# Kernel optimization log

Hardware: AMD Instinct MI355X
Metric: run time of the kernel (lower is better)

The kernel has to match this reference:

```python
import jax, jax.numpy as jnp
import numpy as np

CX, CY, FX, FY = 334.081, 169.808, 460.585, 460.268
EPS = 1e-07
T_ITER = 1000
MIN_POINTS = 5000
H, W, B = 360, 640, 2


def _point_cloud(depth_img):
    # depth_img: [C,H,W]; channel 2 if C==3 else channel 0
    depth = depth_img[2] if depth_img.shape[0] == 3 else depth_img[0]
    rows, cols = depth.shape
    c = jnp.arange(cols, dtype=depth.dtype)[None, :]
    r = jnp.arange(rows, dtype=depth.dtype)[:, None]
    valid = (depth > 0) & (depth < 65535)
    nanv = jnp.float32(jnp.nan)
    z = jnp.where(valid, depth / 1000.0, nanv)
    x = jnp.where(valid, z * (c - CX) / FX, nanv)
    y = jnp.where(valid, z * (r - CY) / FY, nanv)
    pcd = jnp.stack([x.ravel(), y.ravel(), z.ravel()], axis=1)  # [N,3]
    return pcd, valid.ravel()


def setup_inputs() -> dict:
    key = jax.random.key(0)
    k1, k2 = jax.random.split(key)
    fake = jax.random.uniform(k1, (B, 1, H, W), dtype=jnp.float32)
    real = jax.random.uniform(k2, (B, 1, H, W), dtype=jnp.float32)
    return {"fake": fake, "real": real, "epoch": 5, "show_image": 0}


def _forward(fake, real, epoch):
    real_pcd, vr = _point_cloud(real[0])
    fake_pcd, vf = _point_cloud(fake[0])
    real_pcd = real_pcd * 1000.0
    fake_pcd = fake_pcd * 1000.0
    # pcd[pcd==0] = eps  (NaN==0 is False, NaNs preserved)
    real_pcd = jnp.where(real_pcd == 0, EPS, real_pcd)
    fake_pcd = jnp.where(fake_pcd == 0, EPS, fake_pcd)

    # combined validity mask (real-valid then fake-valid filtering chain)
    m = vr & vf
    cnt = jnp.maximum(jnp.sum(m), 1)

    def sel(v, fill):
        return jnp.where(m, v, fill)

    def mrmse(a, b):
        d = sel(a, 0.0) - sel(b, 0.0)
        return jnp.sqrt(jnp.sum(d * d) / cnt)

    lossX = mrmse(real_pcd[:, 0], fake_pcd[:, 0])
    lossY = mrmse(real_pcd[:, 1], fake_pcd[:, 1])
    lossZ = mrmse(real_pcd[:, 2], fake_pcd[:, 2])
    dlog = jnp.log(jnp.abs(sel(real_pcd[:, 2], 1.0))) - jnp.log(jnp.abs(sel(fake_pcd[:, 2], 1.0)))
    RMSE_log = 10000.0 * jnp.sqrt(jnp.sum(jnp.where(m, dlog * dlog, 0.0)) / cnt)
    loss17 = RMSE_log * jnp.abs(10.0 * (3.0 - jnp.exp(lossX) - jnp.exp(lossY) - jnp.exp(lossZ)))

    # ---- batched RANSAC plane fit on normalized fake cloud ----
    nan_cloud = jnp.where(jnp.isnan(fake_pcd), 0.0, fake_pcd)
    pts = nan_cloud / jnp.max(nan_cloud)  # [N,3]
    N = pts.shape[0]
    thresh = jnp.maximum(jnp.float32(0.025 - 0.001 * epoch), jnp.float32(0.005))

    rkey = jax.random.key(42)
    idx = jax.random.randint(rkey, (T_ITER, 3), 0, N)  # 3 sample points per trial
    p = pts[idx]  # [T,3,3]
    vA = p[:, 1] - p[:, 0]
    vB = p[:, 2] - p[:, 0]
    nrm = jnp.cross(vA, vB)
    nrm = nrm / jnp.linalg.norm(nrm, axis=1, keepdims=True)  # unit normals [T,3]
    kk = -jnp.sum(nrm * p[:, 1], axis=1)  # plane offsets [T]
    dist = pts @ nrm.T + kk[None, :]  # [N,T], |n|=1 so no extra divide
    inl = jnp.abs(dist) <= thresh  # [N,T]
    counts = jnp.sum(inl, axis=0)  # [T]
    # keep first trial with strictly-largest count among counts > minPoints
    score = jnp.where(counts > MIN_POINTS, counts, -1)
    best = jnp.argmax(score)
    a, b, c, d = nrm[best, 0], nrm[best, 1], nrm[best, 2], kk[best]
    inlier_mask = inl[:, best]  # [N]

    # translation/rotation were built via torch.tensor(...) -> detached in torch
    trans = jax.lax.stop_gradient(jnp.stack([jnp.zeros(()), jnp.zeros(()), d / c]))
    n2 = a * a + b * b + c * c
    cos_t = c / jnp.sqrt(n2)
    sin_t = jnp.sqrt((a * a + b * b) / n2)
    sab = jnp.sqrt(a * a + b * b)
    u1 = b / sab
    u2 = -a / sab
    R = jnp.stack([
        jnp.stack([cos_t + u1 * u1 * (1 - cos_t), u1 * u2 * (1 - cos_t), u2 * sin_t]),
        jnp.stack([u1 * u2 * (1 - cos_t), cos_t + u2 * u2 * (1 - cos_t), -u1 * sin_t]),
        jnp.stack([-u2 * sin_t, u1 * sin_t, cos_t]),
    ])
    Rt = jax.lax.stop_gradient(R).T  # torch transposes before matmul

    plane_pts = pts + trans
    zc = (plane_pts @ Rt)[:, 2]  # rotated z for all points; inliers selected by mask
    icnt = jnp.maximum(jnp.sum(inlier_mask), 1)
    zmax = jnp.max(jnp.where(inlier_mask, zc, -jnp.inf))
    zmin = jnp.min(jnp.where(inlier_mask, zc, jnp.inf))
    below = jnp.sum(jnp.where(inlier_mask, jnp.abs(zc - zmax), 0.0)) / icnt
    above = jnp.sum(jnp.where(inlier_mask, jnp.abs(zc - zmin), 0.0)) / icnt
    above = jnp.where(above == 0, jnp.float32(1e-07), above)
    plane_mean_dist_grad = 1000.0 * (above + below)

    loss_curv = loss17 + plane_mean_dist_grad
    delta = jnp.stack([RMSE_log, lossX, lossY, lossZ, plane_mean_dist_grad, loss17])
    return delta, loss_curv


def reference(fake, real, epoch, show_image):
    del show_image  # unused in the loss math
    return _forward(fake, real, epoch)
```

## Files before the change

kernel.cpp:

```cpp
#include <hip/hip_runtime.h>

namespace {

typedef float v2f __attribute__((ext_vector_type(2)));

constexpr int kW = 640;
constexpr int kN = 230400;
constexpr unsigned kSpan = 230400u;
constexpr int kB1 = 900;
constexpr int kB3 = 1024;
constexpr int kPPB3 = 225;
constexpr int kB5 = 900;
constexpr unsigned kPoison = 0xAAAAAAAAu;

struct __align__(16) Acc {
  double lossX, lossY, lossZ, rmse_log, loss17;
  float maxv;
  unsigned selkey;
};

constexpr size_t kOffAcc     = 0;
constexpr size_t kOffC1      = 256;
constexpr size_t kOffC3      = 320;
constexpr size_t kOffC5      = 384;
constexpr size_t kOffPlanes  = 512;
constexpr size_t kOffSP      = 512 + 16384;
constexpr size_t kOffZP      = kOffSP + 43200;
constexpr size_t kOffPartial = kOffZP + 28800;
constexpr size_t kOffPts     = kOffPartial + (size_t)kB3 * 256 * 4;

__device__ __forceinline__ void ast64(unsigned long long* p, unsigned long long v) {
  __hip_atomic_store(p, v, __ATOMIC_RELAXED, __HIP_MEMORY_SCOPE_AGENT);
}
__device__ __forceinline__ unsigned long long ald64(const unsigned long long* p) {
  return __hip_atomic_load(p, __ATOMIC_RELAXED, __HIP_MEMORY_SCOPE_AGENT);
}
__device__ __forceinline__ void ast32(unsigned* p, unsigned v) {
  __hip_atomic_store(p, v, __ATOMIC_RELAXED, __HIP_MEMORY_SCOPE_AGENT);
}
__device__ __forceinline__ unsigned ald32(const unsigned* p) {
  return __hip_atomic_load(p, __ATOMIC_RELAXED, __HIP_MEMORY_SCOPE_AGENT);
}

__device__ __forceinline__ unsigned rotl32(unsigned v, int r) {
  return (v << r) | (v >> (32 - r));
}

__device__ __forceinline__ void threefry(unsigned c0, unsigned c1,
                                         unsigned& o0, unsigned& o1) {
  const unsigned ks0 = 0u, ks1 = 42u, ks2 = 0x1BD11BDAu ^ 0u ^ 42u;
  unsigned x0 = c0 + ks0, x1 = c1 + ks1;
#define TFR(r) { x0 += x1; x1 = rotl32(x1, (r)); x1 ^= x0; }
  TFR(13) TFR(15) TFR(26) TFR(6)
  x0 += ks1; x1 += ks2 + 1u;
  TFR(17) TFR(29) TFR(16) TFR(24)
  x0 += ks2; x1 += ks0 + 2u;
  TFR(13) TFR(15) TFR(26) TFR(6)
  x0 += ks0; x1 += ks1 + 3u;
  TFR(17) TFR(29) TFR(16) TFR(24)
  x0 += ks1; x1 += ks2 + 4u;
  TFR(13) TFR(15) TFR(26) TFR(6)
  x0 += ks2; x1 += ks0 + 5u;
#undef TFR
  o0 = x0; o1 = x1;
}

__device__ __forceinline__ void pix_coords(float d, int row, int col, bool& valid,
                                           float& x, float& y, float& z) {
  valid = (d > 0.0f) && (d < 65535.0f);
  float z0 = d / 1000.0f;
  float x0 = z0 * ((float)col - 334.081f) / 460.585f;
  float y0 = z0 * ((float)row - 169.808f) / 460.268f;
  x = x0 * 1000.0f;
  y = y0 * 1000.0f;
  z = z0 * 1000.0f;
  if (x == 0.0f) x = 1e-7f;
  if (y == 0.0f) y = 1e-7f;
  if (z == 0.0f) z = 1e-7f;
}

__device__ __forceinline__ void make_pt(float d, int row, int col, float maxv,
                                        float& x, float& y, float& z) {
  bool v; float a, b, c;
  pix_coords(d, row, col, v, a, b, c);
  x = (v ? a : 0.f) / maxv;
  y = (v ? b : 0.f) / maxv;
  z = (v ? c : 0.f) / maxv;
}

__device__ __forceinline__ float get_thresh(int ep) {
  return (float)fmax(0.025 - 0.001 * (double)ep, 0.005);
}

__global__ __launch_bounds__(256) void k_stats(const float* __restrict__ fake,
                                               const float* __restrict__ real,
                                               float* __restrict__ out,
                                               char* __restrict__ ws) {
  Acc* acc = (Acc*)(ws + kOffAcc);
  unsigned* ctr = (unsigned*)(ws + kOffC1);
  float4* planes = (float4*)(ws + kOffPlanes);
  unsigned long long* sp = (unsigned long long*)(ws + kOffSP);
  float4* ptsraw = (float4*)(ws + kOffPts);

  const int b = blockIdx.x, t = threadIdx.x;
  const int lane = t & 63, wid = t >> 6;

  __shared__ double sD0[4], sD1[4], sD2[4], sD3[4];
  __shared__ int sI0[4];
  __shared__ float sF0[4];
  __shared__ unsigned sArr;
  __shared__ float sMaxv;

  {
    int i = b * 256 + t;
    int row = i / kW, col = i - row * kW;
    bool vr, vf; float rx, ry, rz, fx, fy, fz;
    pix_coords(real[i], row, col, vr, rx, ry, rz);
    pix_coords(fake[i], row, col, vf, fx, fy, fz);
    ptsraw[i] = make_float4(vf ? fx : 0.f, vf ? fy : 0.f, vf ? fz : 0.f, 0.f);
    double dx2 = 0, dy2 = 0, dz2 = 0, dl2 = 0; int cc = 0;
    if (vr && vf) {
      float ddx = rx - fx, ddy = ry - fy, ddz = rz - fz;
      dx2 = (double)ddx * (double)ddx;
      dy2 = (double)ddy * (double)ddy;
      dz2 = (double)ddz * (double)ddz;
      double dl = log(fabs((double)rz)) - log(fabs((double)fz));
      dl2 = dl * dl;
      cc = 1;
    }
    float mx = vf ? fmaxf(fmaxf(fx, fy), fz) : 0.0f;
    for (int o = 32; o; o >>= 1) {
      dx2 += __shfl_down(dx2, o); dy2 += __shfl_down(dy2, o);
      dz2 += __shfl_down(dz2, o); dl2 += __shfl_down(dl2, o);
      cc += __shfl_down(cc, o);
      mx = fmaxf(mx, __shfl_down(mx, o));
    }
    if (lane == 0) { sD0[wid]=dx2; sD1[wid]=dy2; sD2[wid]=dz2; sD3[wid]=dl2;
                     sI0[wid]=cc; sF0[wid]=mx; }
    __syncthreads();
    if (t == 0) {
      unsigned long long* e = sp + (size_t)b * 6;
      ast64(e + 0, __double_as_longlong(sD0[0]+sD0[1]+sD0[2]+sD0[3]));
      ast64(e + 1, __double_as_longlong(sD1[0]+sD1[1]+sD1[2]+sD1[3]));
      ast64(e + 2, __double_as_longlong(sD2[0]+sD2[1]+sD2[2]+sD2[3]));
      ast64(e + 3, __double_as_longlong(sD3[0]+sD3[1]+sD3[2]+sD3[3]));
      ast64(e + 4, (unsigned long long)(sI0[0]+sI0[1]+sI0[2]+sI0[3]));
      float bm = fmaxf(fmaxf(sF0[0], sF0[1]), fmaxf(sF0[2], sF0[3]));
      ast64(e + 5, (unsigned long long)__float_as_uint(bm));
    }
  }
  __syncthreads();
  if (t == 0)
    sArr = __hip_atomic_fetch_add(ctr, 1u, __ATOMIC_RELAXED, __HIP_MEMORY_SCOPE_AGENT);
  __syncthreads();
  if (sArr != kPoison + (unsigned)(kB1 - 1)) return;

  {
    double gx = 0, gy = 0, gz = 0, gl = 0; int gc = 0; float gm = 0.f;
    for (int r = t; r < kB1; r += 256) {
      const unsigned long long* e = sp + (size_t)r * 6;
      gx += __longlong_as_double(ald64(e + 0));
      gy += __longlong_as_double(ald64(e + 1));
      gz += __longlong_as_double(ald64(e + 2));
      gl += __longlong_as_double(ald64(e + 3));
      gc += (int)ald64(e + 4);
      gm = fmaxf(gm, __uint_as_float((unsigned)ald64(e + 5)));
    }
    for (int o = 32; o; o >>= 1) {
      gx += __shfl_down(gx, o); gy += __shfl_down(gy, o);
      gz += __shfl_down(gz, o); gl += __shfl_down(gl, o);
      gc += __shfl_down(gc, o);
      gm = fmaxf(gm, __shfl_down(gm, o));
    }
    if (lane == 0) { sD0[wid]=gx; sD1[wid]=gy; sD2[wid]=gz; sD3[wid]=gl;
                     sI0[wid]=gc; sF0[wid]=gm; }
    __syncthreads();
    if (t == 0) {
      double SX = sD0[0]+sD0[1]+sD0[2]+sD0[3];
      double SY = sD1[0]+sD1[1]+sD1[2]+sD1[3];
      double SZ = sD2[0]+sD2[1]+sD2[2]+sD2[3];
      double SL = sD3[0]+sD3[1]+sD3[2]+sD3[3];
      int CN = sI0[0]+sI0[1]+sI0[2]+sI0[3];
      float MX = fmaxf(fmaxf(sF0[0], sF0[1]), fmaxf(sF0[2], sF0[3]));
      double cntd = (CN > 0) ? (double)CN : 1.0;
      double lossX = sqrt(SX / cntd);
      double lossY = sqrt(SY / cntd);
      double lossZ = sqrt(SZ / cntd);
      double rmse_log = 10000.0 * sqrt(SL / cntd);
      double loss17 = rmse_log * fabs(10.0 * (3.0 - exp(lossX) - exp(lossY) - exp(lossZ)));
      acc->lossX = lossX; acc->lossY = lossY; acc->lossZ = lossZ;
      acc->rmse_log = rmse_log; acc->loss17 = loss17;
      acc->maxv = MX;
      acc->selkey = 0u;
      out[0] = (float)rmse_log;
      out[1] = (float)lossX;
      out[2] = (float)lossY;
      out[3] = (float)lossZ;
      out[5] = (float)loss17;
      sMaxv = MX;
    }
    __syncthreads();
  }
  {
    float maxv = sMaxv;
#pragma unroll
    for (int j = 0; j < 4; j++) {
      int pid = t * 4 + j;
      if (pid < 1000) {
        float px[3], py[3], pz[3];
#pragma unroll
        for (int v = 0; v < 3; v++) {
          unsigned p = 3u * (unsigned)pid + (unsigned)v;
          unsigned o0, o1;
          threefry(p, p + 3000u, o0, o1);
          unsigned idx = o1 % kSpan;
          int row = (int)(idx / kW), col = (int)idx - row * kW;
          make_pt(fake[idx], row, col, maxv, px[v], py[v], pz[v]);
        }
        float ax = px[1]-px[0], ay = py[1]-py[0], az = pz[1]-pz[0];
        float bx = px[2]-px[0], by = py[2]-py[0], bz = pz[2]-pz[0];
        float nx = ay*bz - az*by;
        float ny = az*bx - ax*bz;
        float nz = ax*by - ay*bx;
        float nn = sqrtf(nx*nx + ny*ny + nz*nz);
        nx /= nn; ny /= nn; nz /= nn;
        float kk = -(nx*px[1] + ny*py[1] + nz*pz[1]);
        planes[pid] = make_float4(nx, ny, nz, kk);
      } else {
        planes[pid] = make_float4(0.f, 0.f, 0.f, 3e38f);
      }
    }
  }
}

__global__ __launch_bounds__(256) void k_count(const int* __restrict__ epoch,
                                               char* __restrict__ ws) {
  Acc* acc = (Acc*)(ws + kOffAcc);
  unsigned* ctr = (unsigned*)(ws + kOffC3);
  const float4* planes = (const float4*)(ws + kOffPlanes);
  unsigned* partial = (unsigned*)(ws + kOffPartial);
  const float4* ptsraw = (const float4*)(ws + kOffPts);

  const int b = blockIdx.x, t = threadIdx.x;
  const float th = get_thresh(*epoch);
  const float maxv = acc->maxv;

  __shared__ float4 sPts[kPPB3];
  __shared__ uint4 sAcc[16][16];
  __shared__ unsigned sArr;

  if (t < kPPB3) {
    float4 r = ptsraw[b * kPPB3 + t];
    sPts[t] = make_float4(r.x / maxv, r.y / maxv, r.z / maxv, 0.f);
  }
  float4 p0 = planes[t * 4 + 0], p1 = planes[t * 4 + 1];
  float4 p2 = planes[t * 4 + 2], p3 = planes[t * 4 + 3];
  v2f Ax = {p0.x, p1.x}, Ay = {p0.y, p1.y}, Az = {p0.z, p1.z}, Aw = {p0.w, p1.w};
  v2f Bx = {p2.x, p3.x}, By = {p2.y, p3.y}, Bz = {p2.z, p3.z}, Bw = {p2.w, p3.w};
  __syncthreads();

  int c0 = 0, c1 = 0, c2 = 0, c3 = 0;
#pragma unroll 5
  for (int s = 0; s < kPPB3; ++s) {
    float4 q = sPts[s];
    v2f qx = {q.x, q.x}, qy = {q.y, q.y}, qz = {q.z, q.z};
    v2f dA = __builtin_elementwise_fma(qx, Ax,
             __builtin_elementwise_fma(qy, Ay,
             __builtin_elementwise_fma(qz, Az, Aw)));
    v2f dB = __builtin_elementwise_fma(qx, Bx,
             __builtin_elementwise_fma(qy, By,
             __builtin_elementwise_fma(qz, Bz, Bw)));
    c0 += (fabsf(dA.x) <= th) ? 1 : 0;
    c1 += (fabsf(dA.y) <= th) ? 1 : 0;
    c2 += (fabsf(dB.x) <= th) ? 1 : 0;
    c3 += (fabsf(dB.y) <= th) ? 1 : 0;
  }
  ast32(&partial[b * 256 + t],
        (unsigned)c0 | ((unsigned)c1 << 8) | ((unsigned)c2 << 16) | ((unsigned)c3 << 24));

  __syncthreads();
  if (t == 0)
    sArr = __hip_atomic_fetch_add(ctr, 1u, __ATOMIC_RELAXED, __HIP_MEMORY_SCOPE_AGENT);
  __syncthreads();
  unsigned ret = sArr;
  if (ret < kPoison + (unsigned)(kB3 - 16)) return;

  int r = (int)(ret - (kPoison + (unsigned)(kB3 - 16)));
  if (t == 0) {
    while (ald32(ctr) != kPoison + (unsigned)kB3) __builtin_amdgcn_s_sleep(2);
  }
  __syncthreads();

  int owner = r * 16 + (t & 15);
  int chunk = t >> 4;
  unsigned s0 = 0, s1 = 0, s2 = 0, s3 = 0;
  for (int row = chunk * 64; row < chunk * 64 + 64; ++row) {
    unsigned v = ald32(&partial[row * 256 + owner]);
    s0 += v & 0xFFu; s1 += (v >> 8) & 0xFFu;
    s2 += (v >> 16) & 0xFFu; s3 += (v >> 24) & 0xFFu;
  }
  sAcc[t & 15][chunk] = make_uint4(s0, s1, s2, s3);
  __syncthreads();

  unsigned mykey = 0u;
  if (t < 16) {
    unsigned t0 = 0, t1 = 0, t2 = 0, t3 = 0;
    for (int j = 0; j < 16; ++j) {
      uint4 v = sAcc[t][j];
      t0 += v.x; t1 += v.y; t2 += v.z; t3 += v.w;
    }
    unsigned tot[4] = {t0, t1, t2, t3};
    int pbase = (r * 16 + t) * 4;
#pragma unroll
    for (int k = 0; k < 4; ++k) {
      int p = pbase + k;
      if (p < 1000) {
        int score = ((int)tot[k] > 5000) ? (int)tot[k] : -1;
        unsigned key = ((unsigned)(score + 2) << 10) | (unsigned)(1023 - p);
        mykey = key > mykey ? key : mykey;
      }
    }
  }
  for (int o = 32; o; o >>= 1) {
    unsigned other = __shfl_down(mykey, o);
    mykey = other > mykey ? other : mykey;
  }
  if (t == 0) atomicMax(&acc->selkey, mykey);
}

__global__ __launch_bounds__(256) void k_zc(const int* __restrict__ epoch,
                                            float* __restrict__ out,
                                            char* __restrict__ ws) {
  Acc* acc = (Acc*)(ws + kOffAcc);
  unsigned* ctr = (unsigned*)(ws + kOffC5);
  const float4* planes = (const float4*)(ws + kOffPlanes);
  unsigned long long* zp = (unsigned long long*)(ws + kOffZP);
  const float4* ptsraw = (const float4*)(ws + kOffPts);

  const int b = blockIdx.x, t = threadIdx.x;
  const int lane = t & 63, wid = t >> 6;
  const float th = get_thresh(*epoch);
  const float maxv = acc->maxv;

  int best = 1023 - (int)(acc->selkey & 1023u);
  float4 pl = planes[best];
  const float a = pl.x, bb = pl.y, c = pl.z, d = pl.w;
  float n2 = a * a + bb * bb + c * c;
  float cos_t = c / sqrtf(n2);
  float sin_t = sqrtf((a * a + bb * bb) / n2);
  float sab = sqrtf(a * a + bb * bb);
  float u1 = bb / sab, u2 = -a / sab;
  const float r0 = -u2 * sin_t, r1 = u1 * sin_t, r2 = cos_t, tz = d / c;

  __shared__ double sD0[4];
  __shared__ int sI0[4];
  __shared__ float sF0[4], sF1[4];
  __shared__ unsigned sArr;

  double sz = 0.0; int ic = 0; float zmx = -INFINITY, zmn = -INFINITY;
  {
    float4 rw = ptsraw[b * 256 + t];
    float qx = rw.x / maxv, qy = rw.y / maxv, qz = rw.z / maxv;
    float dist = fmaf(qx, a, fmaf(qy, bb, fmaf(qz, c, d)));
    if (fabsf(dist) <= th) {
      float zc = fmaf(qx, r0, fmaf(qy, r1, (qz + tz) * r2));
      sz = (double)zc; ic = 1; zmx = zc; zmn = -zc;
    }
  }
  for (int o = 32; o; o >>= 1) {
    sz += __shfl_down(sz, o); ic += __shfl_down(ic, o);
    zmx = fmaxf(zmx, __shfl_down(zmx, o));
    zmn = fmaxf(zmn, __shfl_down(zmn, o));
  }
  if (lane == 0) { sD0[wid] = sz; sI0[wid] = ic; sF0[wid] = zmx; sF1[wid] = zmn; }
  __syncthreads();
  if (t == 0) {
    unsigned long long* e = zp + (size_t)b * 4;
    ast64(e + 0, __double_as_longlong(sD0[0]+sD0[1]+sD0[2]+sD0[3]));
    ast64(e + 1, (unsigned long long)(sI0[0]+sI0[1]+sI0[2]+sI0[3]));
    float bmx = fmaxf(fmaxf(sF0[0], sF0[1]), fmaxf(sF0[2], sF0[3]));
    float bmn = fmaxf(fmaxf(sF1[0], sF1[1]), fmaxf(sF1[2], sF1[3]));
    ast64(e + 2, (unsigned long long)__float_as_uint(bmx) |
                 ((unsigned long long)__float_as_uint(bmn) << 32));
  }
  __syncthreads();
  if (t == 0)
    sArr = __hip_atomic_fetch_add(ctr, 1u, __ATOMIC_RELAXED, __HIP_MEMORY_SCOPE_AGENT);
  __syncthreads();
  if (sArr != kPoison + (unsigned)(kB5 - 1)) return;

  {
    double gs = 0.0; int gi = 0; float gmx = -INFINITY, gmn = -INFINITY;
    for (int r = t; r < kB5; r += 256) {
      const unsigned long long* e = zp + (size_t)r * 4;
      gs += __longlong_as_double(ald64(e + 0));
      gi += (int)ald64(e + 1);
      unsigned long long mm = ald64(e + 2);
      gmx = fmaxf(gmx, __uint_as_float((unsigned)(mm & 0xFFFFFFFFu)));
      gmn = fmaxf(gmn, __uint_as_float((unsigned)(mm >> 32)));
    }
    for (int o = 32; o; o >>= 1) {
      gs += __shfl_down(gs, o); gi += __shfl_down(gi, o);
      gmx = fmaxf(gmx, __shfl_down(gmx, o));
      gmn = fmaxf(gmn, __shfl_down(gmn, o));
    }
    if (lane == 0) { sD0[wid] = gs; sI0[wid] = gi; sF0[wid] = gmx; sF1[wid] = gmn; }
    __syncthreads();
    if (t == 0) {
      double S = sD0[0]+sD0[1]+sD0[2]+sD0[3];
      int IC = sI0[0]+sI0[1]+sI0[2]+sI0[3];
      float MX = fmaxf(fmaxf(sF0[0], sF0[1]), fmaxf(sF0[2], sF0[3]));
      float MN = fmaxf(fmaxf(sF1[0], sF1[1]), fmaxf(sF1[2], sF1[3]));
      double below = 0.0, above = 0.0;
      if (IC > 0) {
        double icd = (double)IC;
        double mean = S / icd;
        below = (double)MX - mean;
        above = mean - (double)(-MN);
      }
      if (above == 0.0) above = 1e-7;
      double pmdg = 1000.0 * (above + below);
      out[4] = (float)pmdg;
      out[6] = (float)(acc->loss17 + pmdg);
    }
  }
}

}

extern "C" void kernel_launch(void* const* d_in, const int* in_sizes, int n_in,
                              void* d_out, int out_size, void* d_ws, size_t ws_size,
                              hipStream_t stream) {
  (void)in_sizes; (void)n_in; (void)out_size; (void)ws_size;
  const float* fake = (const float*)d_in[0];
  const float* real = (const float*)d_in[1];
  const int* epoch = (const int*)d_in[2];
  float* out = (float*)d_out;
  char* ws = (char*)d_ws;

  k_stats<<<kB1, 256, 0, stream>>>(fake, real, out, ws);
  k_count<<<kB3, 256, 0, stream>>>(epoch, ws);
  k_zc<<<kB5, 256, 0, stream>>>(epoch, out, ws);
}
```

Before: 135.6 us.

## Fuse three kernels into one persistent kernel with grid-wide flag synchronization

Merges the stats, RANSAC inlier-count and plane-z kernels into one kernel of 512 blocks, each owning 450 pixels kept in shared memory across all phases. The global point buffer and two extra launches go away. Blocks now spin on global flags (plane-ready, selection-done), so the design relies on all 512 blocks being co-resident, with launch bounds set to two blocks per SM. Partial counts are widened to 16-bit fields since each block now covers more points.

```diff
diff --git a/kernel.cpp b/kernel.cpp
--- a/kernel.cpp
+++ b/kernel.cpp
@@ -5,29 +5,21 @@
 typedef float v2f __attribute__((ext_vector_type(2)));
 
 constexpr int kW = 640;
-constexpr int kN = 230400;
 constexpr unsigned kSpan = 230400u;
-constexpr int kB1 = 900;
-constexpr int kB3 = 1024;
-constexpr int kPPB3 = 225;
-constexpr int kB5 = 900;
+constexpr int kB = 512;
+constexpr int kPPB = 450;
 constexpr unsigned kPoison = 0xAAAAAAAAu;
 
-struct __align__(16) Acc {
-  double lossX, lossY, lossZ, rmse_log, loss17;
-  float maxv;
-  unsigned selkey;
-};
-
 constexpr size_t kOffAcc     = 0;
-constexpr size_t kOffC1      = 256;
-constexpr size_t kOffC3      = 320;
-constexpr size_t kOffC5      = 384;
-constexpr size_t kOffPlanes  = 512;
-constexpr size_t kOffSP      = 512 + 16384;
-constexpr size_t kOffZP      = kOffSP + 43200;
-constexpr size_t kOffPartial = kOffZP + 28800;
-constexpr size_t kOffPts     = kOffPartial + (size_t)kB3 * 256 * 4;
+constexpr size_t kOffCA      = 256;
+constexpr size_t kOffCB      = 320;
+constexpr size_t kOffCSel    = 384;
+constexpr size_t kOffCC      = 448;
+constexpr size_t kOffFlagPl  = 512;
+constexpr size_t kOffPlanes  = 1024;
+constexpr size_t kOffSP      = kOffPlanes + 16384;
+constexpr size_t kOffZP      = kOffSP + 24576;
+constexpr size_t kOffPartial = kOffZP + 16384;
 
 __device__ __forceinline__ void ast64(unsigned long long* p, unsigned long long v) {
   __hip_atomic_store(p, v, __ATOMIC_RELAXED, __HIP_MEMORY_SCOPE_AGENT);
@@ -40,6 +32,23 @@
 }
 __device__ __forceinline__ unsigned ald32(const unsigned* p) {
   return __hip_atomic_load(p, __ATOMIC_RELAXED, __HIP_MEMORY_SCOPE_AGENT);
+}
+__device__ __forceinline__ void ast32rel(unsigned* p, unsigned v) {
+  __hip_atomic_store(p, v, __ATOMIC_RELEASE, __HIP_MEMORY_SCOPE_AGENT);
+}
+__device__ __forceinline__ unsigned ald32acq(const unsigned* p) {
+  return __hip_atomic_load(p, __ATOMIC_ACQUIRE, __HIP_MEMORY_SCOPE_AGENT);
+}
+
+__device__ __forceinline__ float lo_f(unsigned long long v) {
+  return __uint_as_float((unsigned)(v & 0xFFFFFFFFull));
+}
+__device__ __forceinline__ float hi_f(unsigned long long v) {
+  return __uint_as_float((unsigned)(v >> 32));
+}
+__device__ __forceinline__ unsigned long long pack_f2(float lo, float hi) {
+  return (unsigned long long)__float_as_uint(lo) |
+         ((unsigned long long)__float_as_uint(hi) << 32);
 }
 
 __device__ __forceinline__ unsigned rotl32(unsigned v, int r) {
@@ -92,43 +101,57 @@
   return (float)fmax(0.025 - 0.001 * (double)ep, 0.005);
 }
 
-__global__ __launch_bounds__(256) void k_stats(const float* __restrict__ fake,
-                                               const float* __restrict__ real,
-                                               float* __restrict__ out,
-                                               char* __restrict__ ws) {
-  Acc* acc = (Acc*)(ws + kOffAcc);
-  unsigned* ctr = (unsigned*)(ws + kOffC1);
-  float4* planes = (float4*)(ws + kOffPlanes);
+__global__ __launch_bounds__(256, 2) void k_fused(const float* __restrict__ fake,
+                                                  const float* __restrict__ real,
+                                                  const int* __restrict__ epoch,
+                                                  float* __restrict__ out,
+                                                  char* __restrict__ ws) {
+  unsigned* maxvBits = (unsigned*)(ws + kOffAcc);
+  unsigned long long* loss17p = (unsigned long long*)(ws + kOffAcc + 8);
+  unsigned* selkeyp = (unsigned*)(ws + kOffAcc + 16);
+  unsigned* ctrA = (unsigned*)(ws + kOffCA);
+  unsigned* ctrB = (unsigned*)(ws + kOffCB);
+  unsigned* ctrSel = (unsigned*)(ws + kOffCSel);
+  unsigned* ctrC = (unsigned*)(ws + kOffCC);
+  unsigned* flagPl = (unsigned*)(ws + kOffFlagPl);
+  unsigned long long* planes64 = (unsigned long long*)(ws + kOffPlanes);
   unsigned long long* sp = (unsigned long long*)(ws + kOffSP);
-  float4* ptsraw = (float4*)(ws + kOffPts);
+  unsigned long long* zp = (unsigned long long*)(ws + kOffZP);
+  unsigned long long* partial = (unsigned long long*)(ws + kOffPartial);
 
   const int b = blockIdx.x, t = threadIdx.x;
   const int lane = t & 63, wid = t >> 6;
-
+  const float th = get_thresh(*epoch);
+
+  __shared__ float4 sPts[kPPB];
   __shared__ double sD0[4], sD1[4], sD2[4], sD3[4];
   __shared__ int sI0[4];
-  __shared__ float sF0[4];
+  __shared__ float sF0[4], sF1[4];
+  __shared__ uint4 sAcc[16][16];
   __shared__ unsigned sArr;
   __shared__ float sMaxv;
+  __shared__ unsigned long long sPl[2];
 
   {
-    int i = b * 256 + t;
-    int row = i / kW, col = i - row * kW;
-    bool vr, vf; float rx, ry, rz, fx, fy, fz;
-    pix_coords(real[i], row, col, vr, rx, ry, rz);
-    pix_coords(fake[i], row, col, vf, fx, fy, fz);
-    ptsraw[i] = make_float4(vf ? fx : 0.f, vf ? fy : 0.f, vf ? fz : 0.f, 0.f);
-    double dx2 = 0, dy2 = 0, dz2 = 0, dl2 = 0; int cc = 0;
-    if (vr && vf) {
-      float ddx = rx - fx, ddy = ry - fy, ddz = rz - fz;
-      dx2 = (double)ddx * (double)ddx;
-      dy2 = (double)ddy * (double)ddy;
-      dz2 = (double)ddz * (double)ddz;
-      double dl = log(fabs((double)rz)) - log(fabs((double)fz));
-      dl2 = dl * dl;
-      cc = 1;
-    }
-    float mx = vf ? fmaxf(fmaxf(fx, fy), fz) : 0.0f;
+    double dx2 = 0, dy2 = 0, dz2 = 0, dl2 = 0; int cc = 0; float mx = 0.f;
+    for (int k = t; k < kPPB; k += 256) {
+      const int i = b * kPPB + k;
+      const int row = i / kW, col = i - row * kW;
+      bool vr, vf; float rx, ry, rz, fxx, fyy, fzz;
+      pix_coords(real[i], row, col, vr, rx, ry, rz);
+      pix_coords(fake[i], row, col, vf, fxx, fyy, fzz);
+      sPts[k] = make_float4(vf ? fxx : 0.f, vf ? fyy : 0.f, vf ? fzz : 0.f, 0.f);
+      if (vr && vf) {
+        float ddx = rx - fxx, ddy = ry - fyy, ddz = rz - fzz;
+        dx2 += (double)ddx * (double)ddx;
+        dy2 += (double)ddy * (double)ddy;
+        dz2 += (double)ddz * (double)ddz;
+        double dl = log(fabs((double)rz)) - log(fabs((double)fzz));
+        dl2 += dl * dl;
+        cc += 1;
+      }
+      mx = fmaxf(mx, vf ? fmaxf(fmaxf(fxx, fyy), fzz) : 0.f);
+    }
     for (int o = 32; o; o >>= 1) {
       dx2 += __shfl_down(dx2, o); dy2 += __shfl_down(dy2, o);
       dz2 += __shfl_down(dz2, o); dl2 += __shfl_down(dl2, o);
@@ -151,247 +174,245 @@
   }
   __syncthreads();
   if (t == 0)
-    sArr = __hip_atomic_fetch_add(ctr, 1u, __ATOMIC_RELAXED, __HIP_MEMORY_SCOPE_AGENT);
-  __syncthreads();
-  if (sArr != kPoison + (unsigned)(kB1 - 1)) return;
+    sArr = __hip_atomic_fetch_add(ctrA, 1u, __ATOMIC_RELAXED, __HIP_MEMORY_SCOPE_AGENT);
+  __syncthreads();
+
+  if (sArr == kPoison + (unsigned)(kB - 1)) {
+    {
+      double gx = 0, gy = 0, gz = 0, gl = 0; int gc = 0; float gm = 0.f;
+      for (int r = t; r < kB; r += 256) {
+        const unsigned long long* e = sp + (size_t)r * 6;
+        gx += __longlong_as_double(ald64(e + 0));
+        gy += __longlong_as_double(ald64(e + 1));
+        gz += __longlong_as_double(ald64(e + 2));
+        gl += __longlong_as_double(ald64(e + 3));
+        gc += (int)ald64(e + 4);
+        gm = fmaxf(gm, __uint_as_float((unsigned)ald64(e + 5)));
+      }
+      for (int o = 32; o; o >>= 1) {
+        gx += __shfl_down(gx, o); gy += __shfl_down(gy, o);
+        gz += __shfl_down(gz, o); gl += __shfl_down(gl, o);
+        gc += __shfl_down(gc, o);
+        gm = fmaxf(gm, __shfl_down(gm, o));
+      }
+      if (lane == 0) { sD0[wid]=gx; sD1[wid]=gy; sD2[wid]=gz; sD3[wid]=gl;
+                       sI0[wid]=gc; sF0[wid]=gm; }
+      __syncthreads();
+      if (t == 0) {
+        double SX = sD0[0]+sD0[1]+sD0[2]+sD0[3];
+        double SY = sD1[0]+sD1[1]+sD1[2]+sD1[3];
+        double SZ = sD2[0]+sD2[1]+sD2[2]+sD2[3];
+        double SL = sD3[0]+sD3[1]+sD3[2]+sD3[3];
+        int CN = sI0[0]+sI0[1]+sI0[2]+sI0[3];
+        float MX = fmaxf(fmaxf(sF0[0], sF0[1]), fmaxf(sF0[2], sF0[3]));
+        double cntd = (CN > 0) ? (double)CN : 1.0;
+        double lossX = sqrt(SX / cntd);
+        double lossY = sqrt(SY / cntd);
+        double lossZ = sqrt(SZ / cntd);
+        double rmse_log = 10000.0 * sqrt(SL / cntd);
+        double loss17 = rmse_log * fabs(10.0 * (3.0 - exp(lossX) - exp(lossY) - exp(lossZ)));
+        ast32(maxvBits, __float_as_uint(MX));
+        ast64(loss17p, __double_as_longlong(loss17));
+        ast32(selkeyp, 0u);
+        out[0] = (float)rmse_log;
+        out[1] = (float)lossX;
+        out[2] = (float)lossY;
+        out[3] = (float)lossZ;
+        out[5] = (float)loss17;
+        sMaxv = MX;
+      }
+      __syncthreads();
+    }
+    {
+      float maxv = sMaxv;
+#pragma unroll
+      for (int j = 0; j < 4; j++) {
+        int pid = t * 4 + j;
+        if (pid < 1000) {
+          float px[3], py[3], pz[3];
+#pragma unroll
+          for (int v = 0; v < 3; v++) {
+            unsigned p = 3u * (unsigned)pid + (unsigned)v;
+            unsigned o0, o1;
+            threefry(p, p + 3000u, o0, o1);
+            unsigned idx = o1 % kSpan;
+            int row = (int)(idx / kW), col = (int)idx - row * kW;
+            make_pt(fake[idx], row, col, maxv, px[v], py[v], pz[v]);
+          }
+          float ax = px[1]-px[0], ay = py[1]-py[0], az = pz[1]-pz[0];
+          float bx = px[2]-px[0], by = py[2]-py[0], bz = pz[2]-pz[0];
+          float nx = ay*bz - az*by;
+          float ny = az*bx - ax*bz;
+          float nz = ax*by - ay*bx;
+          float nn = sqrtf(nx*nx + ny*ny + nz*nz);
+          nx /= nn; ny /= nn; nz /= nn;
+          float kk = -(nx*px[1] + ny*py[1] + nz*pz[1]);
+          ast64(planes64 + 2*pid,     pack_f2(nx, ny));
+          ast64(planes64 + 2*pid + 1, pack_f2(nz, kk));
+        } else {
+          ast64(planes64 + 2*pid,     pack_f2(0.f, 0.f));
+          ast64(planes64 + 2*pid + 1, pack_f2(0.f, 3e38f));
+        }
+      }
+    }
+    __syncthreads();
+    if (t == 0) ast32rel(flagPl, 1u);
+  }
+
+  if (t == 0) {
+    while (ald32acq(flagPl) != 1u) __builtin_amdgcn_s_sleep(2);
+    sMaxv = __uint_as_float(ald32(maxvBits));
+  }
+  __syncthreads();
+  const float maxv = sMaxv;
 
   {
-    double gx = 0, gy = 0, gz = 0, gl = 0; int gc = 0; float gm = 0.f;
-    for (int r = t; r < kB1; r += 256) {
-      const unsigned long long* e = sp + (size_t)r * 6;
-      gx += __longlong_as_double(ald64(e + 0));
-      gy += __longlong_as_double(ald64(e + 1));
-      gz += __longlong_as_double(ald64(e + 2));
-      gl += __longlong_as_double(ald64(e + 3));
-      gc += (int)ald64(e + 4);
-      gm = fmaxf(gm, __uint_as_float((unsigned)ald64(e + 5)));
+    float4 pl[4];
+#pragma unroll
+    for (int j = 0; j < 4; j++) {
+      unsigned long long w0 = ald64(planes64 + 2 * (t * 4 + j));
+      unsigned long long w1 = ald64(planes64 + 2 * (t * 4 + j) + 1);
+      pl[j] = make_float4(lo_f(w0), hi_f(w0), lo_f(w1), hi_f(w1));
+    }
+    for (int k = t; k < kPPB; k += 256) {
+      float4 r = sPts[k];
+      sPts[k] = make_float4(r.x / maxv, r.y / maxv, r.z / maxv, 0.f);
+    }
+    v2f Ax = {pl[0].x, pl[1].x}, Ay = {pl[0].y, pl[1].y},
+        Az = {pl[0].z, pl[1].z}, Aw = {pl[0].w, pl[1].w};
+    v2f Bx = {pl[2].x, pl[3].x}, By = {pl[2].y, pl[3].y},
+        Bz = {pl[2].z, pl[3].z}, Bw = {pl[2].w, pl[3].w};
+    __syncthreads();
+
+    int c0 = 0, c1 = 0, c2 = 0, c3 = 0;
+#pragma unroll 5
+    for (int s = 0; s < kPPB; ++s) {
+      float4 q = sPts[s];
+      v2f qx = {q.x, q.x}, qy = {q.y, q.y}, qz = {q.z, q.z};
+      v2f dA = __builtin_elementwise_fma(qx, Ax,
+               __builtin_elementwise_fma(qy, Ay,
+               __builtin_elementwise_fma(qz, Az, Aw)));
+      v2f dB = __builtin_elementwise_fma(qx, Bx,
+               __builtin_elementwise_fma(qy, By,
+               __builtin_elementwise_fma(qz, Bz, Bw)));
+      c0 += (fabsf(dA.x) <= th) ? 1 : 0;
+      c1 += (fabsf(dA.y) <= th) ? 1 : 0;
+      c2 += (fabsf(dB.x) <= th) ? 1 : 0;
+      c3 += (fabsf(dB.y) <= th) ? 1 : 0;
+    }
+    ast64(&partial[(size_t)b * 256 + t],
+          (unsigned long long)(unsigned)c0 |
+          ((unsigned long long)(unsigned)c1 << 16) |
+          ((unsigned long long)(unsigned)c2 << 32) |
+          ((unsigned long long)(unsigned)c3 << 48));
+  }
+  __syncthreads();
+  if (t == 0)
+    sArr = __hip_atomic_fetch_add(ctrB, 1u, __ATOMIC_RELAXED, __HIP_MEMORY_SCOPE_AGENT);
+  __syncthreads();
+  {
+    unsigned ret = sArr;
+    if (ret >= kPoison + (unsigned)(kB - 16)) {
+      int r = (int)(ret - (kPoison + (unsigned)(kB - 16)));
+      if (t == 0) {
+        while (ald32(ctrB) != kPoison + (unsigned)kB) __builtin_amdgcn_s_sleep(2);
+      }
+      __syncthreads();
+
+      int owner = r * 16 + (t & 15);
+      int chunk = t >> 4;
+      unsigned s0 = 0, s1 = 0, s2 = 0, s3 = 0;
+      for (int row = chunk * 32; row < chunk * 32 + 32; ++row) {
+        unsigned long long v = ald64(&partial[(size_t)row * 256 + owner]);
+        s0 += (unsigned)(v & 0xFFFFu);         s1 += (unsigned)((v >> 16) & 0xFFFFu);
+        s2 += (unsigned)((v >> 32) & 0xFFFFu); s3 += (unsigned)((v >> 48) & 0xFFFFu);
+      }
+      sAcc[t & 15][chunk] = make_uint4(s0, s1, s2, s3);
+      __syncthreads();
+
+      unsigned mykey = 0u;
+      if (t < 16) {
+        unsigned t0 = 0, t1 = 0, t2 = 0, t3 = 0;
+        for (int j = 0; j < 16; ++j) {
+          uint4 v = sAcc[t][j];
+          t0 += v.x; t1 += v.y; t2 += v.z; t3 += v.w;
+        }
+        unsigned tot[4] = {t0, t1, t2, t3};
+        int pbase = (r * 16 + t) * 4;
+#pragma unroll
+        for (int k = 0; k < 4; ++k) {
+          int p = pbase + k;
+          if (p < 1000) {
+            int score = ((int)tot[k] > 5000) ? (int)tot[k] : -1;
+            unsigned key = ((unsigned)(score + 2) << 10) | (unsigned)(1023 - p);
+            mykey = key > mykey ? key : mykey;
+          }
+        }
+      }
+      for (int o = 32; o; o >>= 1) {
+        unsigned other = __shfl_down(mykey, o);
+        mykey = other > mykey ? other : mykey;
+      }
+      if (t == 0) {
+        atomicMax(selkeyp, mykey);
+        __hip_atomic_fetch_add(ctrSel, 1u, __ATOMIC_RELEASE, __HIP_MEMORY_SCOPE_AGENT);
+      }
+    }
+  }
+  if (t == 0) {
+    while (ald32acq(ctrSel) != kPoison + 16u) __builtin_amdgcn_s_sleep(2);
+    unsigned sk = ald32(selkeyp);
+    int best = 1023 - (int)(sk & 1023u);
+    sPl[0] = ald64(planes64 + 2 * best);
+    sPl[1] = ald64(planes64 + 2 * best + 1);
+  }
+  __syncthreads();
+
+  {
+    const float a = lo_f(sPl[0]), bb = hi_f(sPl[0]);
+    const float c = lo_f(sPl[1]), d = hi_f(sPl[1]);
+    float n2 = a * a + bb * bb + c * c;
+    float cos_t = c / sqrtf(n2);
+    float sin_t = sqrtf((a * a + bb * bb) / n2);
+    float sab = sqrtf(a * a + bb * bb);
+    float u1 = bb / sab, u2 = -a / sab;
+    const float r0 = -u2 * sin_t, r1 = u1 * sin_t, r2v = cos_t, tz = d / c;
+
+    double sz = 0.0; int ic = 0; float zmx = -INFINITY, zmn = -INFINITY;
+    for (int k = t; k < kPPB; k += 256) {
+      float4 q = sPts[k];
+      float dist = fmaf(q.x, a, fmaf(q.y, bb, fmaf(q.z, c, d)));
+      if (fabsf(dist) <= th) {
+        float zc = fmaf(q.x, r0, fmaf(q.y, r1, (q.z + tz) * r2v));
+        sz += (double)zc; ic += 1; zmx = fmaxf(zmx, zc); zmn = fmaxf(zmn, -zc);
+      }
     }
     for (int o = 32; o; o >>= 1) {
-      gx += __shfl_down(gx, o); gy += __shfl_down(gy, o);
-      gz += __shfl_down(gz, o); gl += __shfl_down(gl, o);
-      gc += __shfl_down(gc, o);
-      gm = fmaxf(gm, __shfl_down(gm, o));
-    }
-    if (lane == 0) { sD0[wid]=gx; sD1[wid]=gy; sD2[wid]=gz; sD3[wid]=gl;
-                     sI0[wid]=gc; sF0[wid]=gm; }
+      sz += __shfl_down(sz, o); ic += __shfl_down(ic, o);
+      zmx = fmaxf(zmx, __shfl_down(zmx, o));
+      zmn = fmaxf(zmn, __shfl_down(zmn, o));
+    }
+    if (lane == 0) { sD0[wid] = sz; sI0[wid] = ic; sF0[wid] = zmx; sF1[wid] = zmn; }
     __syncthreads();
     if (t == 0) {
-      double SX = sD0[0]+sD0[1]+sD0[2]+sD0[3];
-      double SY = sD1[0]+sD1[1]+sD1[2]+sD1[3];
-      double SZ = sD2[0]+sD2[1]+sD2[2]+sD2[3];
-      double SL = sD3[0]+sD3[1]+sD3[2]+sD3[3];
-      int CN = sI0[0]+sI0[1]+sI0[2]+sI0[3];
-      float MX = fmaxf(fmaxf(sF0[0], sF0[1]), fmaxf(sF0[2], sF0[3]));
-      double cntd = (CN > 0) ? (double)CN : 1.0;
-      double lossX = sqrt(SX / cntd);
-      double lossY = sqrt(SY / cntd);
-      double lossZ = sqrt(SZ / cntd);
-      double rmse_log = 10000.0 * sqrt(SL / cntd);
-      double loss17 = rmse_log * fabs(10.0 * (3.0 - exp(lossX) - exp(lossY) - exp(lossZ)));
-      acc->lossX = lossX; acc->lossY = lossY; acc->lossZ = lossZ;
-      acc->rmse_log = rmse_log; acc->loss17 = loss17;
-      acc->maxv = MX;
-      acc->selkey = 0u;
-      out[0] = (float)rmse_log;
-      out[1] = (float)lossX;
-      out[2] = (float)lossY;
-      out[3] = (float)lossZ;
-      out[5] = (float)loss17;
-      sMaxv = MX;
-    }
-    __syncthreads();
-  }
-  {
-    float maxv = sMaxv;
-#pragma unroll
-    for (int j = 0; j < 4; j++) {
-      int pid = t * 4 + j;
-      if (pid < 1000) {
-        float px[3], py[3], pz[3];
-#pragma unroll
-        for (int v = 0; v < 3; v++) {
-          unsigned p = 3u * (unsigned)pid + (unsigned)v;
-          unsigned o0, o1;
-          threefry(p, p + 3000u, o0, o1);
-          unsigned idx = o1 % kSpan;
-          int row = (int)(idx / kW), col = (int)idx - row * kW;
-          make_pt(fake[idx], row, col, maxv, px[v], py[v], pz[v]);
-        }
-        float ax = px[1]-px[0], ay = py[1]-py[0], az = pz[1]-pz[0];
-        float bx = px[2]-px[0], by = py[2]-py[0], bz = pz[2]-pz[0];
-        float nx = ay*bz - az*by;
-        float ny = az*bx - ax*bz;
-        float nz = ax*by - ay*bx;
-        float nn = sqrtf(nx*nx + ny*ny + nz*nz);
-        nx /= nn; ny /= nn; nz /= nn;
-        float kk = -(nx*px[1] + ny*py[1] + nz*pz[1]);
-        planes[pid] = make_float4(nx, ny, nz, kk);
-      } else {
-        planes[pid] = make_float4(0.f, 0.f, 0.f, 3e38f);
-      }
-    }
-  }
-}
-
-__global__ __launch_bounds__(256) void k_count(const int* __restrict__ epoch,
-                                               char* __restrict__ ws) {
-  Acc* acc = (Acc*)(ws + kOffAcc);
-  unsigned* ctr = (unsigned*)(ws + kOffC3);
-  const float4* planes = (const float4*)(ws + kOffPlanes);
-  unsigned* partial = (unsigned*)(ws + kOffPartial);
-  const float4* ptsraw = (const float4*)(ws + kOffPts);
-
-  const int b = blockIdx.x, t = threadIdx.x;
-  const float th = get_thresh(*epoch);
-  const float maxv = acc->maxv;
-
-  __shared__ float4 sPts[kPPB3];
-  __shared__ uint4 sAcc[16][16];
-  __shared__ unsigned sArr;
-
-  if (t < kPPB3) {
-    float4 r = ptsraw[b * kPPB3 + t];
-    sPts[t] = make_float4(r.x / maxv, r.y / maxv, r.z / maxv, 0.f);
-  }
-  float4 p0 = planes[t * 4 + 0], p1 = planes[t * 4 + 1];
-  float4 p2 = planes[t * 4 + 2], p3 = planes[t * 4 + 3];
-  v2f Ax = {p0.x, p1.x}, Ay = {p0.y, p1.y}, Az = {p0.z, p1.z}, Aw = {p0.w, p1.w};
-  v2f Bx = {p2.x, p3.x}, By = {p2.y, p3.y}, Bz = {p2.z, p3.z}, Bw = {p2.w, p3.w};
-  __syncthreads();
-
-  int c0 = 0, c1 = 0, c2 = 0, c3 = 0;
-#pragma unroll 5
-  for (int s = 0; s < kPPB3; ++s) {
-    float4 q = sPts[s];
-    v2f qx = {q.x, q.x}, qy = {q.y, q.y}, qz = {q.z, q.z};
-    v2f dA = __builtin_elementwise_fma(qx, Ax,
-             __builtin_elementwise_fma(qy, Ay,
-             __builtin_elementwise_fma(qz, Az, Aw)));
-    v2f dB = __builtin_elementwise_fma(qx, Bx,
-             __builtin_elementwise_fma(qy, By,
-             __builtin_elementwise_fma(qz, Bz, Bw)));
-    c0 += (fabsf(dA.x) <= th) ? 1 : 0;
-    c1 += (fabsf(dA.y) <= th) ? 1 : 0;
-    c2 += (fabsf(dB.x) <= th) ? 1 : 0;
-    c3 += (fabsf(dB.y) <= th) ? 1 : 0;
-  }
-  ast32(&partial[b * 256 + t],
-        (unsigned)c0 | ((unsigned)c1 << 8) | ((unsigned)c2 << 16) | ((unsigned)c3 << 24));
-
+      unsigned long long* e = zp + (size_t)b * 4;
+      ast64(e + 0, __double_as_longlong(sD0[0]+sD0[1]+sD0[2]+sD0[3]));
+      ast64(e + 1, (unsigned long long)(sI0[0]+sI0[1]+sI0[2]+sI0[3]));
+      float bmx = fmaxf(fmaxf(sF0[0], sF0[1]), fmaxf(sF0[2], sF0[3]));
+      float bmn = fmaxf(fmaxf(sF1[0], sF1[1]), fmaxf(sF1[2], sF1[3]));
+      ast64(e + 2, (unsigned long long)__float_as_uint(bmx) |
+                   ((unsigned long long)__float_as_uint(bmn) << 32));
+    }
+  }
   __syncthreads();
   if (t == 0)
-    sArr = __hip_atomic_fetch_add(ctr, 1u, __ATOMIC_RELAXED, __HIP_MEMORY_SCOPE_AGENT);
-  __syncthreads();
-  unsigned ret = sArr;
-  if (ret < kPoison + (unsigned)(kB3 - 16)) return;
-
-  int r = (int)(ret - (kPoison + (unsigned)(kB3 - 16)));
-  if (t == 0) {
-    while (ald32(ctr) != kPoison + (unsigned)kB3) __builtin_amdgcn_s_sleep(2);
-  }
-  __syncthreads();
-
-  int owner = r * 16 + (t & 15);
-  int chunk = t >> 4;
-  unsigned s0 = 0, s1 = 0, s2 = 0, s3 = 0;
-  for (int row = chunk * 64; row < chunk * 64 + 64; ++row) {
-    unsigned v = ald32(&partial[row * 256 + owner]);
-    s0 += v & 0xFFu; s1 += (v >> 8) & 0xFFu;
-    s2 += (v >> 16) & 0xFFu; s3 += (v >> 24) & 0xFFu;
-  }
-  sAcc[t & 15][chunk] = make_uint4(s0, s1, s2, s3);
-  __syncthreads();
-
-  unsigned mykey = 0u;
-  if (t < 16) {
-    unsigned t0 = 0, t1 = 0, t2 = 0, t3 = 0;
-    for (int j = 0; j < 16; ++j) {
-      uint4 v = sAcc[t][j];
-      t0 += v.x; t1 += v.y; t2 += v.z; t3 += v.w;
-    }
-    unsigned tot[4] = {t0, t1, t2, t3};
-    int pbase = (r * 16 + t) * 4;
-#pragma unroll
-    for (int k = 0; k < 4; ++k) {
-      int p = pbase + k;
-      if (p < 1000) {
-        int score = ((int)tot[k] > 5000) ? (int)tot[k] : -1;
-        unsigned key = ((unsigned)(score + 2) << 10) | (unsigned)(1023 - p);
-        mykey = key > mykey ? key : mykey;
-      }
-    }
-  }
-  for (int o = 32; o; o >>= 1) {
-    unsigned other = __shfl_down(mykey, o);
-    mykey = other > mykey ? other : mykey;
-  }
-  if (t == 0) atomicMax(&acc->selkey, mykey);
-}
-
-__global__ __launch_bounds__(256) void k_zc(const int* __restrict__ epoch,
-                                            float* __restrict__ out,
-                                            char* __restrict__ ws) {
-  Acc* acc = (Acc*)(ws + kOffAcc);
-  unsigned* ctr = (unsigned*)(ws + kOffC5);
-  const float4* planes = (const float4*)(ws + kOffPlanes);
-  unsigned long long* zp = (unsigned long long*)(ws + kOffZP);
-  const float4* ptsraw = (const float4*)(ws + kOffPts);
-
-  const int b = blockIdx.x, t = threadIdx.x;
-  const int lane = t & 63, wid = t >> 6;
-  const float th = get_thresh(*epoch);
-  const float maxv = acc->maxv;
-
-  int best = 1023 - (int)(acc->selkey & 1023u);
-  float4 pl = planes[best];
-  const float a = pl.x, bb = pl.y, c = pl.z, d = pl.w;
-  float n2 = a * a + bb * bb + c * c;
-  float cos_t = c / sqrtf(n2);
-  float sin_t = sqrtf((a * a + bb * bb) / n2);
-  float sab = sqrtf(a * a + bb * bb);
-  float u1 = bb / sab, u2 = -a / sab;
-  const float r0 = -u2 * sin_t, r1 = u1 * sin_t, r2 = cos_t, tz = d / c;
-
-  __shared__ double sD0[4];
-  __shared__ int sI0[4];
-  __shared__ float sF0[4], sF1[4];
-  __shared__ unsigned sArr;
-
-  double sz = 0.0; int ic = 0; float zmx = -INFINITY, zmn = -INFINITY;
-  {
-    float4 rw = ptsraw[b * 256 + t];
-    float qx = rw.x / maxv, qy = rw.y / maxv, qz = rw.z / maxv;
-    float dist = fmaf(qx, a, fmaf(qy, bb, fmaf(qz, c, d)));
-    if (fabsf(dist) <= th) {
-      float zc = fmaf(qx, r0, fmaf(qy, r1, (qz + tz) * r2));
-      sz = (double)zc; ic = 1; zmx = zc; zmn = -zc;
-    }
-  }
-  for (int o = 32; o; o >>= 1) {
-    sz += __shfl_down(sz, o); ic += __shfl_down(ic, o);
-    zmx = fmaxf(zmx, __shfl_down(zmx, o));
-    zmn = fmaxf(zmn, __shfl_down(zmn, o));
-  }
-  if (lane == 0) { sD0[wid] = sz; sI0[wid] = ic; sF0[wid] = zmx; sF1[wid] = zmn; }
-  __syncthreads();
-  if (t == 0) {
-    unsigned long long* e = zp + (size_t)b * 4;
-    ast64(e + 0, __double_as_longlong(sD0[0]+sD0[1]+sD0[2]+sD0[3]));
-    ast64(e + 1, (unsigned long long)(sI0[0]+sI0[1]+sI0[2]+sI0[3]));
-    float bmx = fmaxf(fmaxf(sF0[0], sF0[1]), fmaxf(sF0[2], sF0[3]));
-    float bmn = fmaxf(fmaxf(sF1[0], sF1[1]), fmaxf(sF1[2], sF1[3]));
-    ast64(e + 2, (unsigned long long)__float_as_uint(bmx) |
-                 ((unsigned long long)__float_as_uint(bmn) << 32));
-  }
-  __syncthreads();
-  if (t == 0)
-    sArr = __hip_atomic_fetch_add(ctr, 1u, __ATOMIC_RELAXED, __HIP_MEMORY_SCOPE_AGENT);
-  __syncthreads();
-  if (sArr != kPoison + (unsigned)(kB5 - 1)) return;
+    sArr = __hip_atomic_fetch_add(ctrC, 1u, __ATOMIC_RELAXED, __HIP_MEMORY_SCOPE_AGENT);
+  __syncthreads();
+  if (sArr != kPoison + (unsigned)(kB - 1)) return;
 
   {
     double gs = 0.0; int gi = 0; float gmx = -INFINITY, gmn = -INFINITY;
-    for (int r = t; r < kB5; r += 256) {
+    for (int r = t; r < kB; r += 256) {
       const unsigned long long* e = zp + (size_t)r * 4;
       gs += __longlong_as_double(ald64(e + 0));
       gi += (int)ald64(e + 1);
@@ -420,8 +441,9 @@
       }
       if (above == 0.0) above = 1e-7;
       double pmdg = 1000.0 * (above + below);
+      double loss17 = __longlong_as_double(ald64(loss17p));
       out[4] = (float)pmdg;
-      out[6] = (float)(acc->loss17 + pmdg);
+      out[6] = (float)(loss17 + pmdg);
     }
   }
 }
@@ -438,7 +460,5 @@
   float* out = (float*)d_out;
   char* ws = (char*)d_ws;
 
-  k_stats<<<kB1, 256, 0, stream>>>(fake, real, out, ws);
-  k_count<<<kB3, 256, 0, stream>>>(epoch, ws);
-  k_zc<<<kB5, 256, 0, stream>>>(epoch, out, ws);
-}
+  k_fused<<<kB, 256, 0, stream>>>(fake, real, epoch, out, ws);
+}
```

New measurement: 205.2 us. 1.51x slower.

## Spread RANSAC plane generation across the last five arriving stats blocks

Applied to the files above, without the earlier changes.

The single last-arriving block in k_stats used to do two serial jobs: the final loss reduction and generating all 1000 candidate planes at four per thread. Now the last five blocks to arrive split this tail. One block does the loss reduction, and the other four each build 256 planes after spin-waiting until every block has arrived. The global max is now gathered with an atomicMax on float bits instead of a per-block slot plus reduction. This relies on the poisoned workspace initial value being a negative int and on all blocks being resident at once for the spin-wait.

```diff
diff --git a/kernel.cpp b/kernel.cpp
--- a/kernel.cpp
+++ b/kernel.cpp
@@ -5,7 +5,6 @@
 typedef float v2f __attribute__((ext_vector_type(2)));
 
 constexpr int kW = 640;
-constexpr int kN = 230400;
 constexpr unsigned kSpan = 230400u;
 constexpr int kB1 = 900;
 constexpr int kB3 = 1024;
@@ -13,13 +12,9 @@
 constexpr int kB5 = 900;
 constexpr unsigned kPoison = 0xAAAAAAAAu;
 
-struct __align__(16) Acc {
-  double lossX, lossY, lossZ, rmse_log, loss17;
-  float maxv;
-  unsigned selkey;
-};
-
-constexpr size_t kOffAcc     = 0;
+constexpr size_t kOffMaxv    = 0;
+constexpr size_t kOffL17     = 8;
+constexpr size_t kOffSel     = 16;
 constexpr size_t kOffC1      = 256;
 constexpr size_t kOffC3      = 320;
 constexpr size_t kOffC5      = 384;
@@ -96,7 +91,9 @@
                                                const float* __restrict__ real,
                                                float* __restrict__ out,
                                                char* __restrict__ ws) {
-  Acc* acc = (Acc*)(ws + kOffAcc);
+  int* maxvBits = (int*)(ws + kOffMaxv);
+  unsigned long long* loss17p = (unsigned long long*)(ws + kOffL17);
+  unsigned* selkeyp = (unsigned*)(ws + kOffSel);
   unsigned* ctr = (unsigned*)(ws + kOffC1);
   float4* planes = (float4*)(ws + kOffPlanes);
   unsigned long long* sp = (unsigned long long*)(ws + kOffSP);
@@ -109,7 +106,7 @@
   __shared__ int sI0[4];
   __shared__ float sF0[4];
   __shared__ unsigned sArr;
-  __shared__ float sMaxv;
+  __shared__ unsigned sMvU;
 
   {
     int i = b * 256 + t;
@@ -146,17 +143,19 @@
       ast64(e + 3, __double_as_longlong(sD3[0]+sD3[1]+sD3[2]+sD3[3]));
       ast64(e + 4, (unsigned long long)(sI0[0]+sI0[1]+sI0[2]+sI0[3]));
       float bm = fmaxf(fmaxf(sF0[0], sF0[1]), fmaxf(sF0[2], sF0[3]));
-      ast64(e + 5, (unsigned long long)__float_as_uint(bm));
+      atomicMax(maxvBits, (int)__float_as_uint(bm));
     }
   }
   __syncthreads();
   if (t == 0)
     sArr = __hip_atomic_fetch_add(ctr, 1u, __ATOMIC_RELAXED, __HIP_MEMORY_SCOPE_AGENT);
   __syncthreads();
-  if (sArr != kPoison + (unsigned)(kB1 - 1)) return;
-
-  {
-    double gx = 0, gy = 0, gz = 0, gl = 0; int gc = 0; float gm = 0.f;
+  unsigned ret = sArr;
+  if (ret < kPoison + (unsigned)(kB1 - 5)) return;
+  int role = (int)(ret - (kPoison + (unsigned)(kB1 - 5)));
+
+  if (role == 4) {
+    double gx = 0, gy = 0, gz = 0, gl = 0; int gc = 0;
     for (int r = t; r < kB1; r += 256) {
       const unsigned long long* e = sp + (size_t)r * 6;
       gx += __longlong_as_double(ald64(e + 0));
@@ -164,16 +163,13 @@
       gz += __longlong_as_double(ald64(e + 2));
       gl += __longlong_as_double(ald64(e + 3));
       gc += (int)ald64(e + 4);
-      gm = fmaxf(gm, __uint_as_float((unsigned)ald64(e + 5)));
     }
     for (int o = 32; o; o >>= 1) {
       gx += __shfl_down(gx, o); gy += __shfl_down(gy, o);
       gz += __shfl_down(gz, o); gl += __shfl_down(gl, o);
       gc += __shfl_down(gc, o);
-      gm = fmaxf(gm, __shfl_down(gm, o));
-    }
-    if (lane == 0) { sD0[wid]=gx; sD1[wid]=gy; sD2[wid]=gz; sD3[wid]=gl;
-                     sI0[wid]=gc; sF0[wid]=gm; }
+    }
+    if (lane == 0) { sD0[wid]=gx; sD1[wid]=gy; sD2[wid]=gz; sD3[wid]=gl; sI0[wid]=gc; }
     __syncthreads();
     if (t == 0) {
       double SX = sD0[0]+sD0[1]+sD0[2]+sD0[3];
@@ -181,61 +177,57 @@
       double SZ = sD2[0]+sD2[1]+sD2[2]+sD2[3];
       double SL = sD3[0]+sD3[1]+sD3[2]+sD3[3];
       int CN = sI0[0]+sI0[1]+sI0[2]+sI0[3];
-      float MX = fmaxf(fmaxf(sF0[0], sF0[1]), fmaxf(sF0[2], sF0[3]));
       double cntd = (CN > 0) ? (double)CN : 1.0;
       double lossX = sqrt(SX / cntd);
       double lossY = sqrt(SY / cntd);
       double lossZ = sqrt(SZ / cntd);
       double rmse_log = 10000.0 * sqrt(SL / cntd);
       double loss17 = rmse_log * fabs(10.0 * (3.0 - exp(lossX) - exp(lossY) - exp(lossZ)));
-      acc->lossX = lossX; acc->lossY = lossY; acc->lossZ = lossZ;
-      acc->rmse_log = rmse_log; acc->loss17 = loss17;
-      acc->maxv = MX;
-      acc->selkey = 0u;
+      ast64(loss17p, __double_as_longlong(loss17));
+      ast32(selkeyp, 0u);
       out[0] = (float)rmse_log;
       out[1] = (float)lossX;
       out[2] = (float)lossY;
       out[3] = (float)lossZ;
       out[5] = (float)loss17;
-      sMaxv = MX;
+    }
+  } else {
+    if (t == 0) {
+      while (ald32(ctr) != kPoison + (unsigned)kB1) __builtin_amdgcn_s_sleep(8);
+      sMvU = ald32((const unsigned*)maxvBits);
     }
     __syncthreads();
-  }
-  {
-    float maxv = sMaxv;
+    const float maxv = __uint_as_float(sMvU);
+    int pid = role * 256 + t;
+    if (pid < 1000) {
+      float px[3], py[3], pz[3];
 #pragma unroll
-    for (int j = 0; j < 4; j++) {
-      int pid = t * 4 + j;
-      if (pid < 1000) {
-        float px[3], py[3], pz[3];
-#pragma unroll
-        for (int v = 0; v < 3; v++) {
-          unsigned p = 3u * (unsigned)pid + (unsigned)v;
-          unsigned o0, o1;
-          threefry(p, p + 3000u, o0, o1);
-          unsigned idx = o1 % kSpan;
-          int row = (int)(idx / kW), col = (int)idx - row * kW;
-          make_pt(fake[idx], row, col, maxv, px[v], py[v], pz[v]);
-        }
-        float ax = px[1]-px[0], ay = py[1]-py[0], az = pz[1]-pz[0];
-        float bx = px[2]-px[0], by = py[2]-py[0], bz = pz[2]-pz[0];
-        float nx = ay*bz - az*by;
-        float ny = az*bx - ax*bz;
-        float nz = ax*by - ay*bx;
-        float nn = sqrtf(nx*nx + ny*ny + nz*nz);
-        nx /= nn; ny /= nn; nz /= nn;
-        float kk = -(nx*px[1] + ny*py[1] + nz*pz[1]);
-        planes[pid] = make_float4(nx, ny, nz, kk);
-      } else {
-        planes[pid] = make_float4(0.f, 0.f, 0.f, 3e38f);
+      for (int v = 0; v < 3; v++) {
+        unsigned p = 3u * (unsigned)pid + (unsigned)v;
+        unsigned o0, o1;
+        threefry(p, p + 3000u, o0, o1);
+        unsigned idx = o1 % kSpan;
+        int row = (int)(idx / kW), col = (int)idx - row * kW;
+        make_pt(fake[idx], row, col, maxv, px[v], py[v], pz[v]);
       }
+      float ax = px[1]-px[0], ay = py[1]-py[0], az = pz[1]-pz[0];
+      float bx = px[2]-px[0], by = py[2]-py[0], bz = pz[2]-pz[0];
+      float nx = ay*bz - az*by;
+      float ny = az*bx - ax*bz;
+      float nz = ax*by - ay*bx;
+      float nn = sqrtf(nx*nx + ny*ny + nz*nz);
+      nx /= nn; ny /= nn; nz /= nn;
+      float kk = -(nx*px[1] + ny*py[1] + nz*pz[1]);
+      planes[pid] = make_float4(nx, ny, nz, kk);
+    } else {
+      planes[pid] = make_float4(0.f, 0.f, 0.f, 3e38f);
     }
   }
 }
 
 __global__ __launch_bounds__(256) void k_count(const int* __restrict__ epoch,
                                                char* __restrict__ ws) {
-  Acc* acc = (Acc*)(ws + kOffAcc);
+  unsigned* selkeyp = (unsigned*)(ws + kOffSel);
   unsigned* ctr = (unsigned*)(ws + kOffC3);
   const float4* planes = (const float4*)(ws + kOffPlanes);
   unsigned* partial = (unsigned*)(ws + kOffPartial);
@@ -243,7 +235,7 @@
 
   const int b = blockIdx.x, t = threadIdx.x;
   const float th = get_thresh(*epoch);
-  const float maxv = acc->maxv;
+  const float maxv = __uint_as_float(*(const unsigned*)(ws + kOffMaxv));
 
   __shared__ float4 sPts[kPPB3];
   __shared__ uint4 sAcc[16][16];
@@ -325,13 +317,13 @@
     unsigned other = __shfl_down(mykey, o);
     mykey = other > mykey ? other : mykey;
   }
-  if (t == 0) atomicMax(&acc->selkey, mykey);
+  if (t == 0) atomicMax(selkeyp, mykey);
 }
 
 __global__ __launch_bounds__(256) void k_zc(const int* __restrict__ epoch,
                                             float* __restrict__ out,
                                             char* __restrict__ ws) {
-  Acc* acc = (Acc*)(ws + kOffAcc);
+  const unsigned long long* loss17p = (const unsigned long long*)(ws + kOffL17);
   unsigned* ctr = (unsigned*)(ws + kOffC5);
   const float4* planes = (const float4*)(ws + kOffPlanes);
   unsigned long long* zp = (unsigned long long*)(ws + kOffZP);
@@ -340,9 +332,10 @@
   const int b = blockIdx.x, t = threadIdx.x;
   const int lane = t & 63, wid = t >> 6;
   const float th = get_thresh(*epoch);
-  const float maxv = acc->maxv;
-
-  int best = 1023 - (int)(acc->selkey & 1023u);
+  const float maxv = __uint_as_float(*(const unsigned*)(ws + kOffMaxv));
+
+  unsigned selkey = *(const unsigned*)(ws + kOffSel);
+  int best = 1023 - (int)(selkey & 1023u);
   float4 pl = planes[best];
   const float a = pl.x, bb = pl.y, c = pl.z, d = pl.w;
   float n2 = a * a + bb * bb + c * c;
@@ -420,8 +413,9 @@
       }
       if (above == 0.0) above = 1e-7;
       double pmdg = 1000.0 * (above + below);
+      double loss17 = __longlong_as_double(ald64(loss17p));
       out[4] = (float)pmdg;
-      out[6] = (float)(acc->loss17 + pmdg);
+      out[6] = (float)(loss17 + pmdg);
     }
   }
 }
```

Result: faster. 129.2 us (-4.7%).
